# Kernel optimization log

Measured on AMD Instinct MI355X. Metric: run time of the kernel, lower is better.

Reference implementation:

```python
import jax, jax.numpy as jnp
import numpy as np

EMBED_DIM = 1024
NUM_HEADS = 16
HEAD_DIM = EMBED_DIM // NUM_HEADS
BSZ, TGT, SRC = 4, 1024, 2048


def setup_inputs() -> dict:
    key = jax.random.key(0)
    ks = jax.random.split(key, 12)
    init = 1.0 / np.sqrt(EMBED_DIM)
    return {
        "hidden_states": jax.random.normal(ks[0], (BSZ, TGT, EMBED_DIM), jnp.float32),
        "key_value_states": jax.random.normal(ks[1], (BSZ, SRC, EMBED_DIM), jnp.float32),
        "bias": jax.random.normal(ks[2], (BSZ, NUM_HEADS, TGT, SRC), jnp.float32),
        "Wq": jax.random.normal(ks[3], (EMBED_DIM, EMBED_DIM), jnp.float32) * init,
        "bq": jax.random.normal(ks[4], (EMBED_DIM,), jnp.float32) * init,
        "Wk": jax.random.normal(ks[5], (EMBED_DIM, EMBED_DIM), jnp.float32) * init,
        "bk": jax.random.normal(ks[6], (EMBED_DIM,), jnp.float32) * init,
        "Wv": jax.random.normal(ks[7], (EMBED_DIM, EMBED_DIM), jnp.float32) * init,
        "bv": jax.random.normal(ks[8], (EMBED_DIM,), jnp.float32) * init,
        "Wo": jax.random.normal(ks[9], (EMBED_DIM, EMBED_DIM), jnp.float32) * init,
        "bo": jax.random.normal(ks[10], (EMBED_DIM,), jnp.float32) * init,
    }


def reference(hidden_states, key_value_states, bias, Wq, bq, Wk, bk, Wv, bv, Wo, bo):
    B, T, E = hidden_states.shape
    S = key_value_states.shape[1]
    H, hd = NUM_HEADS, HEAD_DIM
    scaling = hd ** (-0.5)
    # torch Linear: y = x @ W^T + b
    q = (hidden_states @ Wq.T + bq) * scaling            # [B,T,E]
    k = key_value_states @ Wk.T + bk                     # [B,S,E]
    v = key_value_states @ Wv.T + bv                     # [B,S,E]
    q = q.reshape(B, T, H, hd).transpose(0, 2, 1, 3)     # [B,H,T,hd]
    k = k.reshape(B, S, H, hd).transpose(0, 2, 1, 3)     # [B,H,S,hd]
    v = v.reshape(B, S, H, hd).transpose(0, 2, 1, 3)     # [B,H,S,hd]
    scores = jnp.einsum('bhtd,bhsd->bhts', q, k) + bias  # [B,H,T,S]
    probs = jax.nn.softmax(scores, axis=-1)
    attn = jnp.einsum('bhts,bhsd->bhtd', probs, v)       # [B,H,T,hd]
    # Faithful to the original: reshape (B*H, T, hd) -> (B, T, E) WITHOUT
    # transposing heads back (this is how the torch source does it).
    attn = attn.reshape(B, T, E)
    return attn @ Wo.T + bo
```

## Files before the change

kernel.cpp:

```cpp
#include <hip/hip_runtime.h>

#define DEVI __device__ __forceinline__

typedef __attribute__((ext_vector_type(4))) float f32x4;
typedef __attribute__((ext_vector_type(8))) short bf16x8;

DEVI unsigned short f2bf(float f) {
  unsigned int u = __builtin_bit_cast(unsigned int, f);
  u += 0x7FFFu + ((u >> 16) & 1u);
  return (unsigned short)(u >> 16);
}

DEVI void load_lds16(const void* g, void* l) {
  __builtin_amdgcn_global_load_lds(
      (__attribute__((address_space(1))) void*)g,
      (__attribute__((address_space(3))) void*)l,
      16, 0, 0);
}

DEVI int xcd_swz(int bid, int chunk) { return (bid & 7) * chunk + (bid >> 3); }

struct CvtArgs {
  const float* src[6];
  unsigned short* dst[6];
  int cum[6];
};

__global__ __launch_bounds__(256) void cvt_all(CvtArgs a, int total4) {
  int i = blockIdx.x * 256 + threadIdx.x;
  if (i >= total4) return;
  int s = 0;
#pragma unroll
  for (int k = 1; k < 6; ++k) s += (i >= a.cum[k]);
  const int j = i - a.cum[s];
  const f32x4 v = __builtin_nontemporal_load((const f32x4*)a.src[s] + j);
  ushort4 o;
  o.x = f2bf(v[0]); o.y = f2bf(v[1]); o.z = f2bf(v[2]); o.w = f2bf(v[3]);
  reinterpret_cast<ushort4*>(a.dst[s])[j] = o;
}

template<bool OUT_BF16>
DEVI void gemm_core(const unsigned short* __restrict__ A,
                    const unsigned short* __restrict__ W,
                    const float* __restrict__ bias,
                    void* __restrict__ out,
                    float scale, int log2R,
                    long sb, long st, long sh, long sd,
                    int bx, int by, bool vt)
{
  constexpr int K = 1024;
  __shared__ unsigned short smem[2 * 128 * 64];
  unsigned short* As = smem;
  unsigned short* Bs = smem + 8192;

  const int tid  = threadIdx.x;
  const int wid  = tid >> 6;
  const int lane = tid & 63;
  const int m0 = bx * 128;
  const int n0 = by * 128;
  const int wr = (wid >> 1) * 64;
  const int wc = (wid & 1) * 64;
  const int lg = lane >> 4;
  const int ll = lane & 15;

  f32x4 acc[4][4] = {};

  const char* Ab = (const char*)A + (long)m0 * K * 2;
  const char* Wb = (const char*)W + (long)n0 * K * 2;
  char* AsB = (char*)As;
  char* BsB = (char*)Bs;
  const long rowstride = (long)K * 2;

  for (int kt = 0; kt < K; kt += 64) {
#pragma unroll
    for (int j = 0; j < 4; ++j) {
      const int o    = (wid * 4 + j) * 1024 + lane * 16;
      const int row  = o >> 7;
      const int colb = o & 127;
      load_lds16(Ab + (long)row * rowstride + (long)kt * 2 + colb, AsB + (wid * 4 + j) * 1024);
      load_lds16(Wb + (long)row * rowstride + (long)kt * 2 + colb, BsB + (wid * 4 + j) * 1024);
    }
    __syncthreads();
#pragma unroll
    for (int ks = 0; ks < 2; ++ks) {
      bf16x8 af[4], bfr[4];
#pragma unroll
      for (int i = 0; i < 4; ++i) {
        af[i]  = *(const bf16x8*)&As[(wr + i * 16 + ll) * 64 + ks * 32 + lg * 8];
        bfr[i] = *(const bf16x8*)&Bs[(wc + i * 16 + ll) * 64 + ks * 32 + lg * 8];
      }
#pragma unroll
      for (int i = 0; i < 4; ++i)
#pragma unroll
        for (int j = 0; j < 4; ++j)
          acc[i][j] = __builtin_amdgcn_mfma_f32_16x16x32_bf16(af[i], bfr[j], acc[i][j], 0, 0, 0);
    }
    __syncthreads();
  }

  const int Rmask  = (1 << log2R) - 1;
  const int m_base = m0 + wr;
  const int b   = m_base >> log2R;
  const int tbs = m_base & Rmask;
  const int nn  = n0 + wc;
  float bj[4];
#pragma unroll
  for (int j = 0; j < 4; ++j) bj[j] = bias[nn + j * 16 + ll];

  if (OUT_BF16 && vt) {
    unsigned short* Tw = smem + wid * 2176;
#pragma unroll
    for (int h2 = 0; h2 < 2; ++h2) {
#pragma unroll
      for (int jj = 0; jj < 2; ++jj) {
        const int j = h2 * 2 + jj;
#pragma unroll
        for (int i = 0; i < 4; ++i)
#pragma unroll
          for (int r = 0; r < 4; ++r)
            Tw[(jj * 16 + ll) * 68 + i * 16 + lg * 4 + r] = f2bf((acc[i][j][r] + bj[j]) * scale);
      }
      asm volatile("s_waitcnt lgkmcnt(0)" ::: "memory");
#pragma unroll
      for (int k = 0; k < 8; ++k) {
        const int dloc = k * 4 + lg;
        const int t4   = ll * 4;
        const ushort4 vv = *(const ushort4*)&Tw[dloc * 68 + t4];
        const int n = nn + h2 * 32 + dloc;
        const int h = n >> 6, dd = n & 63;
        *(ushort4*)((unsigned short*)out + (long)b * sb + (long)h * sh + (long)dd * sd + tbs + t4) = vv;
      }
      if (h2 == 0) asm volatile("s_waitcnt lgkmcnt(0)" ::: "memory");
    }
    return;
  }

  if (OUT_BF16) {
    const int h = nn >> 6;
    unsigned short* ob = (unsigned short*)out + (long)b * sb + (long)h * sh;
    unsigned short* Tw = smem + wid * 2176;
#pragma unroll
    for (int p = 0; p < 2; ++p) {
#pragma unroll
      for (int i2 = 0; i2 < 2; ++i2) {
        const int i = p * 2 + i2;
#pragma unroll
        for (int j = 0; j < 4; ++j)
#pragma unroll
          for (int r = 0; r < 4; ++r)
            Tw[(i2 * 16 + lg * 4 + r) * 68 + j * 16 + ll] = f2bf((acc[i][j][r] + bj[j]) * scale);
      }
      asm volatile("s_waitcnt lgkmcnt(0)" ::: "memory");
#pragma unroll
      for (int k = 0; k < 8; ++k) {
        const int t_loc = k * 4 + lg;
        const int d4    = ll * 4;
        const ushort4 vv = *(const ushort4*)&Tw[t_loc * 68 + d4];
        *(ushort4*)(ob + (long)(tbs + p * 32 + t_loc) * st + d4) = vv;
      }
      if (p == 0) asm volatile("s_waitcnt lgkmcnt(0)" ::: "memory");
    }
    return;
  }

  {
    float* ob = (float*)out + (long)b * sb + nn;
    float* TwF = (float*)smem + wid * 1056;
#pragma unroll
    for (int i = 0; i < 4; ++i) {
#pragma unroll
      for (int j = 0; j < 4; ++j)
#pragma unroll
        for (int r = 0; r < 4; ++r)
          TwF[(lg * 4 + r) * 66 + j * 16 + ll] = acc[i][j][r] + bj[j];
      asm volatile("s_waitcnt lgkmcnt(0)" ::: "memory");
#pragma unroll
      for (int k = 0; k < 8; ++k) {
        const int t_loc = k * 2 + (lane >> 5);
        const int c2    = (lane & 31) * 2;
        const float2 v = *(const float2*)&TwF[t_loc * 66 + c2];
        *(float2*)(ob + (long)(tbs + i * 16 + t_loc) * st + c2) = v;
      }
      if (i < 3) asm volatile("s_waitcnt lgkmcnt(0)" ::: "memory");
    }
  }
}

struct GemmDesc {
  const unsigned short* A;
  const unsigned short* W;
  const float* bias;
  unsigned short* out;
  float scale;
  int log2R;
  long sb, st, sh, sd;
};

__global__ __launch_bounds__(256) void gemm_qkv(GemmDesc d0, GemmDesc d1, GemmDesc d2) {
  int bid = xcd_swz(blockIdx.x, 160);
  const GemmDesc* d;
  bool vt = false;
  if (bid < 256)      { d = &d0; }
  else if (bid < 768) { d = &d1; bid -= 256; }
  else                { d = &d2; bid -= 768; vt = true; }
  gemm_core<true>(d->A, d->W, d->bias, d->out, d->scale, d->log2R,
                  d->sb, d->st, d->sh, d->sd, bid >> 3, bid & 7, vt);
}

__global__ __launch_bounds__(256) void gemm_o(
    const unsigned short* __restrict__ A,
    const unsigned short* __restrict__ W,
    const float* __restrict__ bias,
    float* __restrict__ out,
    long sb, long st, long sh, long sd)
{
  const int bid = xcd_swz(blockIdx.x, 32);
  gemm_core<false>(A, W, bias, out, 1.0f, 10, sb, st, sh, sd, bid >> 3, bid & 7, false);
}

__global__ __launch_bounds__(512, 4) void attn_fused(
    const unsigned short* __restrict__ Qb,
    const unsigned short* __restrict__ Kb,
    const unsigned short* __restrict__ Vt,
    const float* __restrict__ bias,
    unsigned short* __restrict__ Ob)
{
  constexpr int T = 1024, S = 2048, NC = S / 64;
  __shared__ unsigned short Ks[64 * 72];
  __shared__ unsigned short Vs[64 * 72];
  __shared__ unsigned short Ps[8][16 * 72];

  const int tid = threadIdx.x;
  const int w = tid >> 6, lane = tid & 63;
  const int lg = lane >> 4, ll = lane & 15;

  const int wg = xcd_swz(blockIdx.x, 64);
  const int bh = wg >> 3;
  const int tt = wg & 7;
  const int t0 = tt * 128;
  const int trow = t0 + w * 16;

  bf16x8 qf[2];
#pragma unroll
  for (int ks = 0; ks < 2; ++ks)
    qf[ks] = *(const bf16x8*)(Qb + ((long)bh * T + trow + ll) * 64 + ks * 32 + lg * 8);

  f32x4 acc[4] = {};
  float m_run = -1e30f, l_run = 0.0f;

  const char* Kg = (const char*)(Kb + (long)bh * S * 64);
  const char* Vg = (const char*)(Vt + (long)bh * 64 * S);
  const float* bias_row = bias + ((long)bh * T + trow + ll) * S + lg * 4;

  const int srow = tid >> 3;
  const int scolb = (tid & 7) * 16;

  f32x4 bA[4], bB[4];
#pragma unroll
  for (int sf = 0; sf < 4; ++sf)
    bA[sf] = __builtin_nontemporal_load((const f32x4*)(bias_row + sf * 16));

  auto body = [&](int sc, f32x4 (&bc)[4], f32x4 (&bn)[4], bool pf) {
    const uint4 kd = *(const uint4*)(Kg + (long)(sc * 64 + srow) * 128 + scolb);
    const uint4 vd = *(const uint4*)(Vg + (long)srow * (S * 2) + sc * 128 + scolb);

    if (pf) {
      const float* bp = bias_row + (sc + 1) * 64;
#pragma unroll
      for (int sf = 0; sf < 4; ++sf)
        bn[sf] = __builtin_nontemporal_load((const f32x4*)(bp + sf * 16));
    }

    *(uint4*)((char*)&Ks[0] + srow * 144 + scolb) = kd;
    *(uint4*)((char*)&Vs[0] + srow * 144 + scolb) = vd;
    asm volatile("s_waitcnt lgkmcnt(0)" ::: "memory");
    __builtin_amdgcn_s_barrier();
    __builtin_amdgcn_sched_barrier(0);

    f32x4 sv[4] = {};
#pragma unroll
    for (int ks = 0; ks < 2; ++ks) {
      bf16x8 kf[4];
#pragma unroll
      for (int sf = 0; sf < 4; ++sf)
        kf[sf] = *(const bf16x8*)((const char*)&Ks[0] + (sf * 16 + ll) * 144 + (ks * 32 + lg * 8) * 2);
#pragma unroll
      for (int sf = 0; sf < 4; ++sf)
        sv[sf] = __builtin_amdgcn_mfma_f32_16x16x32_bf16(kf[sf], qf[ks], sv[sf], 0, 0, 0);
    }

#pragma unroll
    for (int sf = 0; sf < 4; ++sf) {
      sv[sf][0] += bc[sf][0]; sv[sf][1] += bc[sf][1];
      sv[sf][2] += bc[sf][2]; sv[sf][3] += bc[sf][3];
    }

    float cm = sv[0][0];
#pragma unroll
    for (int sf = 0; sf < 4; ++sf)
#pragma unroll
      for (int r = 0; r < 4; ++r) cm = fmaxf(cm, sv[sf][r]);
    cm = fmaxf(cm, __shfl_xor(cm, 16));
    cm = fmaxf(cm, __shfl_xor(cm, 32));

    const float mnew = fmaxf(m_run, cm);
    const float alpha = __expf(m_run - mnew);
    float ps = 0.0f;
#pragma unroll
    for (int sf = 0; sf < 4; ++sf)
#pragma unroll
      for (int r = 0; r < 4; ++r) {
        const float p = __expf(sv[sf][r] - mnew);
        sv[sf][r] = p;
        ps += p;
      }
    ps += __shfl_xor(ps, 16);
    ps += __shfl_xor(ps, 32);
    l_run = l_run * alpha + ps;
    m_run = mnew;

    float ar[4];
#pragma unroll
    for (int r = 0; r < 4; ++r) ar[r] = __shfl(alpha, lg * 4 + r);
#pragma unroll
    for (int df = 0; df < 4; ++df)
#pragma unroll
      for (int r = 0; r < 4; ++r) acc[df][r] *= ar[r];

    unsigned short* Pw = &Ps[w][0];
#pragma unroll
    for (int sf = 0; sf < 4; ++sf) {
      ushort4 pw;
      pw.x = f2bf(sv[sf][0]); pw.y = f2bf(sv[sf][1]);
      pw.z = f2bf(sv[sf][2]); pw.w = f2bf(sv[sf][3]);
      *(ushort4*)&Pw[ll * 72 + sf * 16 + lg * 4] = pw;
    }
    asm volatile("s_waitcnt lgkmcnt(0)" ::: "memory");
    __builtin_amdgcn_sched_barrier(0);

#pragma unroll
    for (int ks = 0; ks < 2; ++ks) {
      bf16x8 pa = *(const bf16x8*)((const char*)Pw + ll * 144 + ks * 64 + lg * 16);
      bf16x8 vf[4];
#pragma unroll
      for (int df = 0; df < 4; ++df)
        vf[df] = *(const bf16x8*)((const char*)&Vs[0] + (df * 16 + ll) * 144 + (ks * 32 + lg * 8) * 2);
#pragma unroll
      for (int df = 0; df < 4; ++df)
        acc[df] = __builtin_amdgcn_mfma_f32_16x16x32_bf16(pa, vf[df], acc[df], 0, 0, 0);
    }
    asm volatile("s_waitcnt lgkmcnt(0)" ::: "memory");
    __builtin_amdgcn_s_barrier();
    __builtin_amdgcn_sched_barrier(0);
  };

  for (int sc = 0; sc < NC; sc += 2) {
    body(sc,     bA, bB, true);
    body(sc + 1, bB, bA, sc + 2 < NC);
  }

  const float inv = 1.0f / l_run;
  float ir[4];
#pragma unroll
  for (int r = 0; r < 4; ++r) ir[r] = __shfl(inv, lg * 4 + r);
#pragma unroll
  for (int df = 0; df < 4; ++df)
#pragma unroll
    for (int r = 0; r < 4; ++r) {
      const long oo = ((long)bh * T + trow + lg * 4 + r) * 64 + df * 16 + ll;
      Ob[oo] = f2bf(acc[df][r] * ir[r]);
    }
}

extern "C" void kernel_launch(void* const* d_in, const int* in_sizes, int n_in,
                              void* d_out, int out_size, void* d_ws, size_t ws_size,
                              hipStream_t stream) {
  constexpr int B = 4, T = 1024, S = 2048, E = 1024;
  const float* hs   = (const float*)d_in[0];
  const float* kv   = (const float*)d_in[1];
  const float* bias = (const float*)d_in[2];
  const float* Wq   = (const float*)d_in[3];
  const float* bq   = (const float*)d_in[4];
  const float* Wk   = (const float*)d_in[5];
  const float* bk   = (const float*)d_in[6];
  const float* Wv   = (const float*)d_in[7];
  const float* bv   = (const float*)d_in[8];
  const float* Wo   = (const float*)d_in[9];
  const float* bo   = (const float*)d_in[10];

  char* ws = (char*)d_ws;
  const size_t MB = 1024 * 1024;
  unsigned short* hs_bf = (unsigned short*)(ws);
  unsigned short* kv_bf = (unsigned short*)(ws + 8 * MB);
  unsigned short* wq_bf = (unsigned short*)(ws + 24 * MB);
  unsigned short* wk_bf = (unsigned short*)(ws + 26 * MB);
  unsigned short* wv_bf = (unsigned short*)(ws + 28 * MB);
  unsigned short* wo_bf = (unsigned short*)(ws + 30 * MB);
  unsigned short* q_buf = (unsigned short*)(ws + 32 * MB);
  unsigned short* k_buf = (unsigned short*)(ws + 40 * MB);
  unsigned short* v_buf = (unsigned short*)(ws + 56 * MB);
  unsigned short* a_buf = (unsigned short*)(ws + 72 * MB);

  CvtArgs ca;
  ca.src[0] = hs;  ca.dst[0] = hs_bf;
  ca.src[1] = kv;  ca.dst[1] = kv_bf;
  ca.src[2] = Wq;  ca.dst[2] = wq_bf;
  ca.src[3] = Wk;  ca.dst[3] = wk_bf;
  ca.src[4] = Wv;  ca.dst[4] = wv_bf;
  ca.src[5] = Wo;  ca.dst[5] = wo_bf;
  const int n4_hs = B * T * E / 4, n4_kv = B * S * E / 4, n4_w = E * E / 4;
  ca.cum[0] = 0;
  ca.cum[1] = n4_hs;
  ca.cum[2] = n4_hs + n4_kv;
  ca.cum[3] = n4_hs + n4_kv + n4_w;
  ca.cum[4] = n4_hs + n4_kv + 2 * n4_w;
  ca.cum[5] = n4_hs + n4_kv + 3 * n4_w;
  const int total4 = n4_hs + n4_kv + 4 * n4_w;
  cvt_all<<<dim3((total4 + 255) / 256), dim3(256), 0, stream>>>(ca, total4);

  GemmDesc dq{hs_bf, wq_bf, bq, q_buf, 0.125f, 10,
              (long)T * E, 64L, (long)T * 64, 1L};
  GemmDesc dk{kv_bf, wk_bf, bk, k_buf, 1.0f, 11,
              (long)S * E, 64L, (long)S * 64, 1L};
  GemmDesc dv{kv_bf, wv_bf, bv, v_buf, 1.0f, 11,
              (long)S * E, 1L, (long)S * 64, (long)S};
  gemm_qkv<<<dim3(1280), 256, 0, stream>>>(dq, dk, dv);

  attn_fused<<<dim3(512), dim3(512), 0, stream>>>(q_buf, k_buf, v_buf, bias, a_buf);

  gemm_o<<<dim3(256), 256, 0, stream>>>(
      a_buf, wo_bf, bo, (float*)d_out,
      (long)T * E, (long)E, 64L, 1L);
}
```

Before: 277.5 us.

## Double-buffer K/V tiles in LDS to cut one barrier per chunk

The attention kernel now keeps two LDS buffers for the K and V tiles and loads the next chunk from global memory into registers while the current chunk is being computed. The earlier version had two barriers per iteration: one after the LDS store and one after compute. Now there is only one per iteration, and global-load latency can overlap with the MFMA work. In exchange the kernel uses more LDS and more registers, which may lower occupancy.

```diff
diff --git a/kernel.cpp b/kernel.cpp
--- a/kernel.cpp
+++ b/kernel.cpp
@@ -226,8 +226,8 @@
     unsigned short* __restrict__ Ob)
 {
   constexpr int T = 1024, S = 2048, NC = S / 64;
-  __shared__ unsigned short Ks[64 * 72];
-  __shared__ unsigned short Vs[64 * 72];
+  __shared__ unsigned short Ks[2][64 * 72];
+  __shared__ unsigned short Vs[2][64 * 72];
   __shared__ unsigned short Ps[8][16 * 72];
 
   const int tid = threadIdx.x;
@@ -237,8 +237,7 @@
   const int wg = xcd_swz(blockIdx.x, 64);
   const int bh = wg >> 3;
   const int tt = wg & 7;
-  const int t0 = tt * 128;
-  const int trow = t0 + w * 16;
+  const int trow = tt * 128 + w * 16;
 
   bf16x8 qf[2];
 #pragma unroll
@@ -251,50 +250,31 @@
   const char* Kg = (const char*)(Kb + (long)bh * S * 64);
   const char* Vg = (const char*)(Vt + (long)bh * 64 * S);
   const float* bias_row = bias + ((long)bh * T + trow + ll) * S + lg * 4;
+  unsigned short* Pw = &Ps[w][0];
 
   const int srow = tid >> 3;
   const int scolb = (tid & 7) * 16;
 
-  f32x4 bA[4], bB[4];
-#pragma unroll
-  for (int sf = 0; sf < 4; ++sf)
-    bA[sf] = __builtin_nontemporal_load((const f32x4*)(bias_row + sf * 16));
-
-  auto body = [&](int sc, f32x4 (&bc)[4], f32x4 (&bn)[4], bool pf) {
-    const uint4 kd = *(const uint4*)(Kg + (long)(sc * 64 + srow) * 128 + scolb);
-    const uint4 vd = *(const uint4*)(Vg + (long)srow * (S * 2) + sc * 128 + scolb);
-
-    if (pf) {
-      const float* bp = bias_row + (sc + 1) * 64;
-#pragma unroll
-      for (int sf = 0; sf < 4; ++sf)
-        bn[sf] = __builtin_nontemporal_load((const f32x4*)(bp + sf * 16));
-    }
-
-    *(uint4*)((char*)&Ks[0] + srow * 144 + scolb) = kd;
-    *(uint4*)((char*)&Vs[0] + srow * 144 + scolb) = vd;
-    asm volatile("s_waitcnt lgkmcnt(0)" ::: "memory");
-    __builtin_amdgcn_s_barrier();
-    __builtin_amdgcn_sched_barrier(0);
-
+  auto loadK = [&](int sc) { return *(const uint4*)(Kg + (long)(sc * 64 + srow) * 128 + scolb); };
+  auto loadV = [&](int sc) { return *(const uint4*)(Vg + (long)srow * (S * 2) + sc * 128 + scolb); };
+
+  auto compute = [&](int cur, f32x4 (&bc)[4]) {
     f32x4 sv[4] = {};
 #pragma unroll
     for (int ks = 0; ks < 2; ++ks) {
       bf16x8 kf[4];
 #pragma unroll
       for (int sf = 0; sf < 4; ++sf)
-        kf[sf] = *(const bf16x8*)((const char*)&Ks[0] + (sf * 16 + ll) * 144 + (ks * 32 + lg * 8) * 2);
+        kf[sf] = *(const bf16x8*)((const char*)&Ks[cur][0] + (sf * 16 + ll) * 144 + (ks * 32 + lg * 8) * 2);
 #pragma unroll
       for (int sf = 0; sf < 4; ++sf)
         sv[sf] = __builtin_amdgcn_mfma_f32_16x16x32_bf16(kf[sf], qf[ks], sv[sf], 0, 0, 0);
     }
-
 #pragma unroll
     for (int sf = 0; sf < 4; ++sf) {
       sv[sf][0] += bc[sf][0]; sv[sf][1] += bc[sf][1];
       sv[sf][2] += bc[sf][2]; sv[sf][3] += bc[sf][3];
     }
-
     float cm = sv[0][0];
 #pragma unroll
     for (int sf = 0; sf < 4; ++sf)
@@ -327,7 +307,6 @@
 #pragma unroll
       for (int r = 0; r < 4; ++r) acc[df][r] *= ar[r];
 
-    unsigned short* Pw = &Ps[w][0];
 #pragma unroll
     for (int sf = 0; sf < 4; ++sf) {
       ushort4 pw;
@@ -344,19 +323,54 @@
       bf16x8 vf[4];
 #pragma unroll
       for (int df = 0; df < 4; ++df)
-        vf[df] = *(const bf16x8*)((const char*)&Vs[0] + (df * 16 + ll) * 144 + (ks * 32 + lg * 8) * 2);
+        vf[df] = *(const bf16x8*)((const char*)&Vs[cur][0] + (df * 16 + ll) * 144 + (ks * 32 + lg * 8) * 2);
 #pragma unroll
       for (int df = 0; df < 4; ++df)
         acc[df] = __builtin_amdgcn_mfma_f32_16x16x32_bf16(pa, vf[df], acc[df], 0, 0, 0);
     }
+  };
+
+  auto rawbar = [&]() {
     asm volatile("s_waitcnt lgkmcnt(0)" ::: "memory");
     __builtin_amdgcn_s_barrier();
     __builtin_amdgcn_sched_barrier(0);
   };
 
+  uint4 kB = loadK(0), vB = loadV(0);
+  *(uint4*)((char*)&Ks[0][0] + srow * 144 + scolb) = kB;
+  *(uint4*)((char*)&Vs[0][0] + srow * 144 + scolb) = vB;
+  uint4 kA = loadK(1), vA = loadV(1);
+  f32x4 bA[4], bB[4];
+#pragma unroll
+  for (int sf = 0; sf < 4; ++sf)
+    bA[sf] = __builtin_nontemporal_load((const f32x4*)(bias_row + sf * 16));
+  rawbar();
+
   for (int sc = 0; sc < NC; sc += 2) {
-    body(sc,     bA, bB, true);
-    body(sc + 1, bB, bA, sc + 2 < NC);
+    {
+      *(uint4*)((char*)&Ks[1][0] + srow * 144 + scolb) = kA;
+      *(uint4*)((char*)&Vs[1][0] + srow * 144 + scolb) = vA;
+      if (sc + 2 < NC) { kB = loadK(sc + 2); vB = loadV(sc + 2); }
+      const float* bp = bias_row + (sc + 1) * 64;
+#pragma unroll
+      for (int sf = 0; sf < 4; ++sf)
+        bB[sf] = __builtin_nontemporal_load((const f32x4*)(bp + sf * 16));
+      compute(0, bA);
+      rawbar();
+    }
+    {
+      if (sc + 2 < NC) {
+        *(uint4*)((char*)&Ks[0][0] + srow * 144 + scolb) = kB;
+        *(uint4*)((char*)&Vs[0][0] + srow * 144 + scolb) = vB;
+        if (sc + 3 < NC) { kA = loadK(sc + 3); vA = loadV(sc + 3); }
+        const float* bp = bias_row + (sc + 2) * 64;
+#pragma unroll
+        for (int sf = 0; sf < 4; ++sf)
+          bA[sf] = __builtin_nontemporal_load((const f32x4*)(bp + sf * 16));
+      }
+      compute(1, bB);
+      rawbar();
+    }
   }
 
   const float inv = 1.0f / l_run;
```

Measured after the change: 298.0 us. 1.07x slower.
